# Performance work log

Hardware: AMD Instinct MI355X
Metric: run time of the kernel (lower is better)

The kernel has to match this reference:

```python
import jax, jax.numpy as jnp
import numpy as np
import math

B, H, N, D = 32, 8, 257, 64  # batch, heads, seq (256 patches + 1), head dim
DIM = H * D
PIX = 256  # 16*16 flattened mask pixels
EPS = 1e-5


def setup_inputs() -> dict:
    key = jax.random.key(0)
    k1, k2, k3 = jax.random.split(key, 3)
    x = jax.random.normal(k1, (B, N, DIM), dtype=jnp.float32)
    msk = jax.random.randint(k2, (B, 16, 16), 0, 128, dtype=jnp.int32)
    W_qkv = jax.random.normal(k3, (3 * DIM, DIM), dtype=jnp.float32) * (DIM ** -0.5)
    # past_kv initialized to identity per head (np.eye tiled in the torch forward)
    past_kv = jnp.broadcast_to(jnp.eye(D, dtype=jnp.float32), (B, H, D, D))
    gn_weight = jnp.ones((H,), dtype=jnp.float32)
    gn_bias = jnp.zeros((H,), dtype=jnp.float32)
    return {"x": x, "msk": msk, "W_qkv": W_qkv, "past_kv": past_kv,
            "gn_weight": gn_weight, "gn_bias": gn_bias}


def _build_mask(msk):
    # msk: [B,16,16] int; zeros replaced by pseudo-random ints in [1,128)
    noise = jax.random.randint(jax.random.key(42), msk.shape, 1, 128, dtype=jnp.int32)
    m = jnp.where(msk == 0, noise, msk).astype(jnp.float32)
    pix = m.reshape(B, PIX, 1)                       # [B,256,1]
    ip = pix @ jnp.swapaxes(pix, 1, 2)               # [B,256,256] outer product
    ip = ip / jnp.max(ip, axis=(1, 2), keepdims=True)
    dec0 = jnp.exp(-5.0 * jnp.linspace(0.0, 1.0, PIX))       # row [256]
    t = jnp.concatenate([jnp.broadcast_to(dec0[None, None, :], (B, 1, PIX)), ip], axis=1)  # [B,257,256]
    dec1 = jnp.exp(-5.0 * jnp.linspace(0.0, 1.0, N))         # col [257]
    t = jnp.concatenate([jnp.broadcast_to(dec1[None, :, None], (B, N, 1)), t], axis=2)     # [B,257,257]
    eye = jnp.eye(N, dtype=bool)
    t = jnp.where(eye, 1.0, t)   # fill_diagonal_(1)
    t = jnp.tril(t)
    return t[:, None, :, :]      # [B,1,N,N] broadcast over heads


def reference(x, msk, W_qkv, past_kv, gn_weight, gn_bias):
    scale = D ** -0.5  # decay_mask == chunk_decay == inner_decay == dim_heads**-0.5
    qkv = x @ W_qkv.T                                # [B,N,3*DIM]
    q, k, v = jnp.split(qkv, 3, axis=-1)
    def heads(t):
        return t.reshape(B, N, H, D).transpose(0, 2, 1, 3)  # b n (h d) -> b h n d
    q, k, v = heads(q), heads(k), heads(v)

    retention = jnp.einsum('bhnd,bhmd->bhnm', q, k) * scale
    weights_before = jax.nn.softmax(retention / math.sqrt(D), axis=-1)

    mask = _build_mask(msk)
    retention = retention * mask
    weights_after = jax.nn.softmax(retention / math.sqrt(D), axis=-1)

    inner_retention = jnp.einsum('bhnm,bhmd->bhnd', retention, v)
    cross_retention = jnp.einsum('bhnd,bhde->bhne', q, past_kv) * scale
    r = inner_retention + cross_retention            # [B,H,N,D]

    # GroupNorm(groups=H, channels=H): normalize each head over (N,D)
    mean = jnp.mean(r, axis=(2, 3), keepdims=True)
    var = jnp.mean((r - mean) ** 2, axis=(2, 3), keepdims=True)
    rn = (r - mean) / jnp.sqrt(var + EPS)
    rn = rn * gn_weight[None, :, None, None] + gn_bias[None, :, None, None]

    output = rn.transpose(0, 2, 1, 3).reshape(B, N, H * D)  # b h n d -> b n (h d)
    return (output, weights_before, weights_after)
```

## Files before the change

kernel.cpp:

```cpp
#include <hip/hip_runtime.h>
#include <stdint.h>

#define WB_OFF   4210688ull
#define WA_OFF   21119232ull

typedef short short8 __attribute__((ext_vector_type(8)));
typedef float floatx4 __attribute__((ext_vector_type(4)));
typedef __attribute__((address_space(1))) const unsigned int gu32;
typedef __attribute__((address_space(3))) unsigned int lu32;

#define RAW_BARRIER() do { \
  __builtin_amdgcn_sched_barrier(0); \
  asm volatile("s_waitcnt lgkmcnt(0)" ::: "memory"); \
  __builtin_amdgcn_s_barrier(); \
  __builtin_amdgcn_sched_barrier(0); \
} while(0)

__device__ __forceinline__ unsigned short f2bf(float f){
  union { float f; uint32_t u; } v; v.f = f;
  uint32_t u = v.u;
  uint32_t r = (u + 0x7FFFu + ((u >> 16) & 1u)) >> 16;
  return (unsigned short)r;
}

__device__ __forceinline__ void threefry(uint32_t k0, uint32_t k1, uint32_t c0, uint32_t c1,
                                         uint32_t& o0, uint32_t& o1){
  const uint32_t ks2 = k0 ^ k1 ^ 0x1BD11BDAu;
  uint32_t x0 = c0 + k0, x1 = c1 + k1;
#define TF_R4(a,b,c,d) \
  x0+=x1; x1=(x1<<(a))|(x1>>(32-(a))); x1^=x0; \
  x0+=x1; x1=(x1<<(b))|(x1>>(32-(b))); x1^=x0; \
  x0+=x1; x1=(x1<<(c))|(x1>>(32-(c))); x1^=x0; \
  x0+=x1; x1=(x1<<(d))|(x1>>(32-(d))); x1^=x0;
  TF_R4(13,15,26,6)  x0+=k1;  x1+=ks2+1u;
  TF_R4(17,29,16,24) x0+=ks2; x1+=k0+2u;
  TF_R4(13,15,26,6)  x0+=k0;  x1+=k1+3u;
  TF_R4(17,29,16,24) x0+=k1;  x1+=ks2+4u;
  TF_R4(13,15,26,6)  x0+=ks2; x1+=k0+5u;
#undef TF_R4
  o0 = x0; o1 = x1;
}

__global__ __launch_bounds__(256) void cvt_prep_kernel(const float* __restrict__ x,
                                                       const float* __restrict__ w,
                                                       unsigned short* __restrict__ xb,
                                                       unsigned short* __restrict__ wb,
                                                       const int* __restrict__ msk,
                                                       float* __restrict__ mnorm){
  __shared__ float sm[256];
  if (blockIdx.x < 4880){
    int i = blockIdx.x*256 + threadIdx.x;
    if (i < 1052672){
      float4 v = ((const float4*)x)[i];
      ushort4 o; o.x=f2bf(v.x); o.y=f2bf(v.y); o.z=f2bf(v.z); o.w=f2bf(v.w);
      ((ushort4*)xb)[i] = o;
    } else if (i < 1249280){
      int j = i - 1052672;
      float4 v = ((const float4*)w)[j];
      ushort4 o; o.x=f2bf(v.x); o.y=f2bf(v.y); o.z=f2bf(v.z); o.w=f2bf(v.w);
      ((ushort4*)wb)[j] = o;
    }
  } else {
    const int b = blockIdx.x - 4880, p = threadIdx.x;
    const int i = b*256 + p;
    uint32_t A0, A1, B0, B1;
    threefry(0u, 42u, 0u, 0u, A0, A1);
    threefry(0u, 42u, 0u, 1u, B0, B1);
    uint32_t h0, h1, l0, l1;
    threefry(A0, A1, 0u, (uint32_t)i, h0, h1);
    threefry(B0, B1, 0u, (uint32_t)i, l0, l1);
    uint32_t hb = h0 ^ h1, lb = l0 ^ l1;
    uint32_t off = ((hb % 127u) * 16u + (lb % 127u)) % 127u;
    int mv = msk[i];
    float m = (mv == 0) ? (float)(1u + off) : (float)mv;
    sm[p] = m; __syncthreads();
    for (int s = 128; s > 0; s >>= 1){
      if (p < s) sm[p] = fmaxf(sm[p], sm[p+s]);
      __syncthreads();
    }
    mnorm[i] = m / sm[0];
  }
}

__global__ __launch_bounds__(256) void qkv_gemm(const unsigned short* __restrict__ xb,
                                                const unsigned short* __restrict__ wb,
                                                unsigned short* __restrict__ qkv){
  __shared__ unsigned short sm2[128*64*2 + 128*8];
  unsigned short* al = sm2;
  unsigned short* bl = sm2 + 128*64;
  unsigned short* c_lds = sm2;
  const int bn = blockIdx.x, bm = blockIdx.y;
  const int tid = threadIdx.x;
  const int wave = tid >> 6, lane = tid & 63;
  const int l16 = lane & 15, lq = lane >> 4;
  const int wm = (wave & 1) * 64, wn = (wave >> 1) * 64;
  const int row0 = tid >> 3;
  const int ccg = ((tid & 7) ^ (row0 & 7)) * 8;
  const int sx = (l16 & 7);
  floatx4 acc[4][4] = {};
  for (int kk = 0; kk < 512; kk += 64){
    #pragma unroll
    for (int p = 0; p < 4; p++){
      int row = p*32 + row0;
      int gm = bm*128 + row; if (gm > 8223) gm = 8223;
      __builtin_amdgcn_global_load_lds((gu32*)&xb[(size_t)gm*512 + kk + ccg],
                                       (lu32*)&al[row*64 + (tid & 7)*8], 16, 0, 0);
      int gn = bn*128 + row;
      __builtin_amdgcn_global_load_lds((gu32*)&wb[(size_t)gn*512 + kk + ccg],
                                       (lu32*)&bl[row*64 + (tid & 7)*8], 16, 0, 0);
    }
    __syncthreads();
    #pragma unroll
    for (int ks = 0; ks < 2; ks++){
      short8 af[4], bf4[4];
      #pragma unroll
      for (int mi = 0; mi < 4; mi++){
        int ch = (ks*4 + lq) ^ sx;
        af[mi] = *(const short8*)&al[(wm + mi*16 + l16)*64 + ch*8];
      }
      #pragma unroll
      for (int ni = 0; ni < 4; ni++){
        int ch = (ks*4 + lq) ^ sx;
        bf4[ni] = *(const short8*)&bl[(wn + ni*16 + l16)*64 + ch*8];
      }
      #pragma unroll
      for (int mi = 0; mi < 4; mi++)
        #pragma unroll
        for (int ni = 0; ni < 4; ni++)
          acc[mi][ni] = __builtin_amdgcn_mfma_f32_16x16x32_bf16(af[mi], bf4[ni], acc[mi][ni], 0, 0, 0);
    }
    __syncthreads();
  }
  #pragma unroll
  for (int mi = 0; mi < 4; mi++)
    #pragma unroll
    for (int ni = 0; ni < 4; ni++)
      #pragma unroll
      for (int r = 0; r < 4; r++)
        c_lds[(wm + mi*16 + lq*4 + r)*136 + wn + ni*16 + l16] = f2bf(acc[mi][ni][r]);
  __syncthreads();
  for (int i = tid; i < 128*16; i += 256){
    int row = i >> 4, cc = (i & 15)*8;
    int gm = bm*128 + row;
    if (gm < 8224){
      ushort4 v0 = *(const ushort4*)&c_lds[row*136 + cc];
      ushort4 v1 = *(const ushort4*)&c_lds[row*136 + cc + 4];
      *(ushort4*)&qkv[(size_t)gm*1536 + bn*128 + cc] = v0;
      *(ushort4*)&qkv[(size_t)gm*1536 + bn*128 + cc + 4] = v1;
    }
  }
}

__global__ __launch_bounds__(256, 3) void retention_kernel(
    const unsigned short* __restrict__ qkv,
    const float* __restrict__ past_kv,
    const float* __restrict__ mnorm,
    float* __restrict__ out,
    float* __restrict__ partials){
  const int id = blockIdx.x;
  const int xcd = id & 7, slot = id >> 3;
  const int w_ = xcd*160 + slot;
  const int t  = w_ % 5;
  const int bh = w_ / 5;
  const int b = bh >> 3, h = bh & 7;
  const int tid = threadIdx.x;
  const int wave = tid >> 6, lane = tid & 63;
  const int l16 = lane & 15, lq = lane >> 4;
  const int rw = wave * 16;

  extern __shared__ unsigned char smem[];
  unsigned short* kl  = (unsigned short*)smem;
  unsigned short* vT  = (unsigned short*)smem;
  unsigned short* pkl = (unsigned short*)(smem + 39168);
  unsigned short* plw = (unsigned short*)(smem + 39168 + wave*1280);
  float* mn  = (float*)(smem + 48384);
  float* red = (float*)(smem + 49408);

  {
    uint32_t* z = (uint32_t*)(kl + 257*72);
    for (int i = tid; i < 540; i += 256) z[i] = 0;
  }
  ushort4 kreg[17];
  #pragma unroll
  for (int u = 0; u < 17; u++){
    int c = tid + u*256;
    if (c < 4112){
      int row = c >> 4, c4 = (c & 15) * 4;
      kreg[u] = *(const ushort4*)&qkv[(size_t)(b*257 + row)*1536 + 512 + h*64 + c4];
    }
  }
  float4 preg[4];
  #pragma unroll
  for (int u = 0; u < 4; u++){
    int c = tid + u*256;
    int d = c >> 4, e4 = (c & 15) * 4;
    preg[u] = *(const float4*)&past_kv[(size_t)bh*4096 + d*64 + e4];
  }
  float mnv = mnorm[b*256 + tid];
  int giA = t*64 + rw + l16; if (giA > 256) giA = 256;
  short8 aq[2];
  aq[0] = *(const short8*)&qkv[(size_t)(b*257 + giA)*1536 + h*64 + lq*8];
  aq[1] = *(const short8*)&qkv[(size_t)(b*257 + giA)*1536 + h*64 + 32 + lq*8];
  ushort4 vreg[17];
  #pragma unroll
  for (int u = 0; u < 17; u++){
    int c = tid + u*256;
    if (c < 4112){
      int row = c >> 4, c4 = (c & 15) * 4;
      vreg[u] = *(const ushort4*)&qkv[(size_t)(b*257 + row)*1536 + 1024 + h*64 + c4];
    }
  }
  #pragma unroll
  for (int u = 0; u < 17; u++){
    int c = tid + u*256;
    if (c < 4112){
      int row = c >> 4, c4 = (c & 15) * 4;
      *(ushort4*)&kl[row*72 + c4] = kreg[u];
    }
  }
  #pragma unroll
  for (int u = 0; u < 4; u++){
    int c = tid + u*256;
    int d = c >> 4, e4 = (c & 15) * 4;
    pkl[(e4+0)*72 + d] = f2bf(0.125f * preg[u].x);
    pkl[(e4+1)*72 + d] = f2bf(0.125f * preg[u].y);
    pkl[(e4+2)*72 + d] = f2bf(0.125f * preg[u].z);
    pkl[(e4+3)*72 + d] = f2bf(0.125f * preg[u].w);
  }
  mn[tid] = mnv;
  RAW_BARRIER();

  floatx4 acc2[4] = {};
  #pragma unroll
  for (int ks = 0; ks < 2; ks++)
    #pragma unroll
    for (int ni = 0; ni < 4; ni++){
      short8 bb = *(const short8*)&pkl[(ni*16 + l16)*72 + ks*32 + lq*8];
      acc2[ni] = __builtin_amdgcn_mfma_f32_16x16x32_bf16(aq[ks], bb, acc2[ni], 0, 0, 0);
    }

  floatx4 acc[17] = {};
  #pragma unroll
  for (int ks = 0; ks < 2; ks++)
    #pragma unroll
    for (int c = 0; c < 17; c++){
      short8 bb = *(const short8*)&kl[(c*16 + l16)*72 + ks*32 + lq*8];
      acc[c] = __builtin_amdgcn_mfma_f32_16x16x32_bf16(aq[ks], bb, acc[c], 0, 0, 0);
    }
  #pragma unroll
  for (int c = 0; c < 17; c++) acc[c] *= 0.125f;

  RAW_BARRIER();

  for (int i = tid; i < 64*19; i += 256){
    int row = i / 19, cc = (i % 19)*2 + 258;
    *(uint32_t*)&vT[row*296 + cc] = 0;
  }
  if (tid < 64) vT[tid*296 + 257] = 0;
  #pragma unroll
  for (int u = 0; u < 17; u++){
    int c = tid + u*256;
    if (c < 4112){
      int row = c >> 4, c4 = (c & 15) * 4;
      vT[(c4+0)*296 + row] = vreg[u].x;
      vT[(c4+1)*296 + row] = vreg[u].y;
      vT[(c4+2)*296 + row] = vreg[u].z;
      vT[(c4+3)*296 + row] = vreg[u].w;
    }
  }
  RAW_BARRIER();

  int gi[4]; bool rowok[4];
  #pragma unroll
  for (int r = 0; r < 4; r++){ gi[r] = t*64 + rw + lq*4 + r; rowok[r] = (gi[r] < 257); }

  float mx[4], sum_[4], inv_[4];

  #pragma unroll
  for (int r = 0; r < 4; r++) mx[r] = -3.0e38f;
  #pragma unroll
  for (int c = 0; c < 17; c++){
    bool jok = (c < 16) || (l16 == 0);
    if (jok){
      #pragma unroll
      for (int r = 0; r < 4; r++) mx[r] = fmaxf(mx[r], acc[c][r]);
    }
  }
  #pragma unroll
  for (int m = 1; m < 16; m <<= 1)
    #pragma unroll
    for (int r = 0; r < 4; r++) mx[r] = fmaxf(mx[r], __shfl_xor(mx[r], m, 64));
  #pragma unroll
  for (int r = 0; r < 4; r++) sum_[r] = 0.f;
  #pragma unroll
  for (int c = 0; c < 17; c++){
    bool jok = (c < 16) || (l16 == 0);
    if (jok){
      #pragma unroll
      for (int r = 0; r < 4; r++) sum_[r] += __expf((acc[c][r] - mx[r]) * 0.125f);
    }
  }
  #pragma unroll
  for (int m = 1; m < 16; m <<= 1)
    #pragma unroll
    for (int r = 0; r < 4; r++) sum_[r] += __shfl_xor(sum_[r], m, 64);
  #pragma unroll
  for (int r = 0; r < 4; r++) inv_[r] = 1.0f / sum_[r];

  {
    const size_t gbase = WB_OFF + (size_t)bh*66049;
    #pragma unroll
    for (int r = 0; r < 4; r++){
      size_t rb = gbase + (size_t)gi[r]*257;
      #pragma unroll
      for (int c = 0; c < 17; c++){
        int j = c*16 + l16;
        if (rowok[r] && j < 257){
          float v = __expf((acc[c][r] - mx[r]) * 0.125f) * inv_[r];
          __builtin_nontemporal_store(v, &out[rb + j]);
        }
      }
    }
  }

  #pragma unroll
  for (int c = 0; c < 17; c++){
    int j = c*16 + l16;
    #pragma unroll
    for (int r = 0; r < 4; r++){
      int ii = gi[r] > 256 ? 256 : gi[r];
      float mv;
      if (j > ii)       mv = 0.f;
      else if (j == ii) mv = 1.f;
      else if (j == 0)  mv = __expf(-5.f * (float)ii * (1.f/256.f));
      else              mv = mn[ii-1] * mn[j-1];
      acc[c][r] *= mv;
    }
  }

  #pragma unroll
  for (int r = 0; r < 4; r++) mx[r] = -3.0e38f;
  #pragma unroll
  for (int c = 0; c < 17; c++){
    bool jok = (c < 16) || (l16 == 0);
    if (jok){
      #pragma unroll
      for (int r = 0; r < 4; r++) mx[r] = fmaxf(mx[r], acc[c][r]);
    }
  }
  #pragma unroll
  for (int m = 1; m < 16; m <<= 1)
    #pragma unroll
    for (int r = 0; r < 4; r++) mx[r] = fmaxf(mx[r], __shfl_xor(mx[r], m, 64));
  #pragma unroll
  for (int r = 0; r < 4; r++) sum_[r] = 0.f;
  #pragma unroll
  for (int c = 0; c < 17; c++){
    bool jok = (c < 16) || (l16 == 0);
    if (jok){
      #pragma unroll
      for (int r = 0; r < 4; r++) sum_[r] += __expf((acc[c][r] - mx[r]) * 0.125f);
    }
  }
  #pragma unroll
  for (int m = 1; m < 16; m <<= 1)
    #pragma unroll
    for (int r = 0; r < 4; r++) sum_[r] += __shfl_xor(sum_[r], m, 64);
  #pragma unroll
  for (int r = 0; r < 4; r++) inv_[r] = 1.0f / sum_[r];

  {
    const size_t gbase = WA_OFF + (size_t)bh*66049;
    #pragma unroll
    for (int r = 0; r < 4; r++){
      size_t rb = gbase + (size_t)gi[r]*257;
      #pragma unroll
      for (int c = 0; c < 17; c++){
        int j = c*16 + l16;
        if (rowok[r] && j < 257){
          float v = __expf((acc[c][r] - mx[r]) * 0.125f) * inv_[r];
          __builtin_nontemporal_store(v, &out[rb + j]);
        }
      }
    }
  }

  const int nks = (t == 4) ? 9 : (2*t + 2);
  #pragma unroll
  for (int ks = 0; ks < 9; ks++){
    if (ks < nks){
      #pragma unroll
      for (int cc = 0; cc < 2; cc++){
        const int f = ks*2 + cc;
        #pragma unroll
        for (int r = 0; r < 4; r++){
          float val = (f < 17 && (f*16 + l16) < 257) ? acc[f][r] : 0.f;
          plw[(lq*4 + r)*40 + cc*16 + l16] = f2bf(val);
        }
      }
      short8 a = *(const short8*)&plw[l16*40 + lq*8];
      #pragma unroll
      for (int ni = 0; ni < 4; ni++){
        short8 bb = *(const short8*)&vT[(ni*16 + l16)*296 + ks*32 + lq*8];
        acc2[ni] = __builtin_amdgcn_mfma_f32_16x16x32_bf16(a, bb, acc2[ni], 0, 0, 0);
      }
    }
  }

  float ls = 0.f, lss = 0.f;
  #pragma unroll
  for (int ni = 0; ni < 4; ni++)
    #pragma unroll
    for (int r = 0; r < 4; r++)
      if (rowok[r]){
        float v = acc2[ni][r];
        ls += v; lss += v*v;
        out[(size_t)(b*257 + gi[r])*512 + h*64 + ni*16 + l16] = v;
      }
  #pragma unroll
  for (int m = 1; m < 64; m <<= 1){ ls += __shfl_xor(ls, m, 64); lss += __shfl_xor(lss, m, 64); }
  if (lane == 0){ red[wave*2] = ls; red[wave*2 + 1] = lss; }
  RAW_BARRIER();
  if (tid == 0){
    partials[((size_t)bh*5 + t)*2 + 0] = red[0] + red[2] + red[4] + red[6];
    partials[((size_t)bh*5 + t)*2 + 1] = red[1] + red[3] + red[5] + red[7];
  }
}

__global__ __launch_bounds__(256) void norm_kernel(const float* __restrict__ partials,
                                                   const float* __restrict__ gnw,
                                                   const float* __restrict__ gnb,
                                                   float* __restrict__ out){
  const int bh = blockIdx.x, b = bh >> 3, h = bh & 7;
  float s = 0.f, s2 = 0.f;
  #pragma unroll
  for (int tt = 0; tt < 5; tt++){
    s  += partials[(bh*5 + tt)*2 + 0];
    s2 += partials[(bh*5 + tt)*2 + 1];
  }
  const float cnt = 257.f * 64.f;
  float mean = s / cnt;
  float var  = s2 / cnt - mean * mean;
  float isd  = rsqrtf(var + 1e-5f);
  float wsc  = gnw[h] * isd;
  float bia  = gnb[h] - mean * wsc;
  for (int idx = threadIdx.x; idx < 257*16; idx += 256){
    int n = idx >> 4, e4 = (idx & 15) * 4;
    size_t off = (size_t)(b*257 + n)*512 + h*64 + e4;
    float4 v = *(float4*)&out[off];
    v.x = v.x * wsc + bia; v.y = v.y * wsc + bia;
    v.z = v.z * wsc + bia; v.w = v.w * wsc + bia;
    *(float4*)&out[off] = v;
  }
}

extern "C" void kernel_launch(void* const* d_in, const int* in_sizes, int n_in,
                              void* d_out, int out_size, void* d_ws, size_t ws_size,
                              hipStream_t stream){
  (void)in_sizes; (void)n_in; (void)out_size; (void)ws_size;
  const float* x   = (const float*)d_in[0];
  const int*   msk = (const int*)d_in[1];
  const float* w   = (const float*)d_in[2];
  const float* pkv = (const float*)d_in[3];
  const float* gnw = (const float*)d_in[4];
  const float* gnb = (const float*)d_in[5];
  float* out = (float*)d_out;

  unsigned short* qkv = (unsigned short*)d_ws;
  unsigned short* xb  = (unsigned short*)((char*)d_ws + 25264128);
  unsigned short* wb  = (unsigned short*)((char*)d_ws + 33685504);
  float* mnorm    = (float*)((char*)d_ws + 35258368);
  float* partials = (float*)((char*)d_ws + 35291136);

  hipLaunchKernelGGL(cvt_prep_kernel, dim3(4912), dim3(256), 0, stream,
                     x, w, xb, wb, msk, mnorm);
  hipLaunchKernelGGL(qkv_gemm, dim3(12, 65), dim3(256), 0, stream, xb, wb, qkv);
  hipLaunchKernelGGL(retention_kernel, dim3(1280), dim3(256), 49440, stream,
                     qkv, pkv, mnorm, out, partials);
  hipLaunchKernelGGL(norm_kernel, dim3(256), dim3(256), 0, stream, partials, gnw, gnb, out);
}
```

Baseline: 265.2 us.

## Stage K in two halves to shrink LDS and allow four blocks per CU

The retention kernel now loads K into LDS in two 128-row halves, with an extra barrier between the halves, instead of all 257 rows at once. The V-transpose stride also drops from 296 to 264, so the shared-memory footprint falls from 49440 to 39968 bytes. Launch bounds go from 3 to 4 blocks per CU to raise occupancy and hide latency. The trade-offs are an extra sync and LDS round, and a tighter register budget that may cause spills given the large kreg, vreg and acc register arrays.

```diff
diff --git a/kernel.cpp b/kernel.cpp
--- a/kernel.cpp
+++ b/kernel.cpp
@@ -151,7 +151,7 @@
   }
 }
 
-__global__ __launch_bounds__(256, 3) void retention_kernel(
+__global__ __launch_bounds__(256, 4) void retention_kernel(
     const unsigned short* __restrict__ qkv,
     const float* __restrict__ past_kv,
     const float* __restrict__ mnorm,
@@ -169,17 +169,13 @@
   const int rw = wave * 16;
 
   extern __shared__ unsigned char smem[];
-  unsigned short* kl  = (unsigned short*)smem;
+  unsigned short* klh = (unsigned short*)smem;
   unsigned short* vT  = (unsigned short*)smem;
-  unsigned short* pkl = (unsigned short*)(smem + 39168);
-  unsigned short* plw = (unsigned short*)(smem + 39168 + wave*1280);
-  float* mn  = (float*)(smem + 48384);
-  float* red = (float*)(smem + 49408);
-
-  {
-    uint32_t* z = (uint32_t*)(kl + 257*72);
-    for (int i = tid; i < 540; i += 256) z[i] = 0;
-  }
+  unsigned short* pkl = (unsigned short*)(smem + 20480);
+  unsigned short* plw = (unsigned short*)(smem + 33792 + wave*1280);
+  float* mn  = (float*)(smem + 38912);
+  float* red = (float*)(smem + 39936);
+
   ushort4 kreg[17];
   #pragma unroll
   for (int u = 0; u < 17; u++){
@@ -211,12 +207,10 @@
     }
   }
   #pragma unroll
-  for (int u = 0; u < 17; u++){
-    int c = tid + u*256;
-    if (c < 4112){
-      int row = c >> 4, c4 = (c & 15) * 4;
-      *(ushort4*)&kl[row*72 + c4] = kreg[u];
-    }
+  for (int u = 0; u < 8; u++){
+    int c = tid + u*256;
+    int row = c >> 4, c4 = (c & 15) * 4;
+    *(ushort4*)&klh[row*72 + c4] = kreg[u];
   }
   #pragma unroll
   for (int u = 0; u < 4; u++){
@@ -243,29 +237,49 @@
   #pragma unroll
   for (int ks = 0; ks < 2; ks++)
     #pragma unroll
-    for (int c = 0; c < 17; c++){
-      short8 bb = *(const short8*)&kl[(c*16 + l16)*72 + ks*32 + lq*8];
+    for (int c = 0; c < 8; c++){
+      short8 bb = *(const short8*)&klh[(c*16 + l16)*72 + ks*32 + lq*8];
       acc[c] = __builtin_amdgcn_mfma_f32_16x16x32_bf16(aq[ks], bb, acc[c], 0, 0, 0);
     }
-  #pragma unroll
-  for (int c = 0; c < 17; c++) acc[c] *= 0.125f;
-
-  RAW_BARRIER();
-
-  for (int i = tid; i < 64*19; i += 256){
-    int row = i / 19, cc = (i % 19)*2 + 258;
-    *(uint32_t*)&vT[row*296 + cc] = 0;
-  }
-  if (tid < 64) vT[tid*296 + 257] = 0;
-  #pragma unroll
-  for (int u = 0; u < 17; u++){
+  RAW_BARRIER();
+
+  #pragma unroll
+  for (int u = 8; u < 17; u++){
     int c = tid + u*256;
     if (c < 4112){
       int row = c >> 4, c4 = (c & 15) * 4;
-      vT[(c4+0)*296 + row] = vreg[u].x;
-      vT[(c4+1)*296 + row] = vreg[u].y;
-      vT[(c4+2)*296 + row] = vreg[u].z;
-      vT[(c4+3)*296 + row] = vreg[u].w;
+      *(ushort4*)&klh[(row-128)*72 + c4] = kreg[u];
+    }
+  }
+  RAW_BARRIER();
+
+  #pragma unroll
+  for (int ks = 0; ks < 2; ks++)
+    #pragma unroll
+    for (int c = 8; c < 17; c++){
+      const int rr = (c == 16) ? 128 : (c*16 - 128);
+      short8 bb = *(const short8*)&klh[(rr + ((c == 16) ? 0 : l16))*72 + ks*32 + lq*8];
+      acc[c] = __builtin_amdgcn_mfma_f32_16x16x32_bf16(aq[ks], bb, acc[c], 0, 0, 0);
+    }
+  #pragma unroll
+  for (int c = 0; c < 17; c++) acc[c] *= 0.125f;
+
+  RAW_BARRIER();
+
+  for (int i = tid; i < 448; i += 256){
+    int r = i / 7, cc = 257 + (i % 7);
+    vT[r*264 + cc] = 0;
+  }
+  if (tid < 16) ((uint32_t*)(smem + 33792))[tid] = 0;
+  #pragma unroll
+  for (int u = 0; u < 17; u++){
+    int c = tid + u*256;
+    if (c < 4112){
+      int row = c >> 4, c4 = (c & 15) * 4;
+      vT[(c4+0)*264 + row] = vreg[u].x;
+      vT[(c4+1)*264 + row] = vreg[u].y;
+      vT[(c4+2)*264 + row] = vreg[u].z;
+      vT[(c4+3)*264 + row] = vreg[u].w;
     }
   }
   RAW_BARRIER();
@@ -401,7 +415,7 @@
       short8 a = *(const short8*)&plw[l16*40 + lq*8];
       #pragma unroll
       for (int ni = 0; ni < 4; ni++){
-        short8 bb = *(const short8*)&vT[(ni*16 + l16)*296 + ks*32 + lq*8];
+        short8 bb = *(const short8*)&vT[(ni*16 + l16)*264 + ks*32 + lq*8];
         acc2[ni] = __builtin_amdgcn_mfma_f32_16x16x32_bf16(a, bb, acc2[ni], 0, 0, 0);
       }
     }
@@ -475,7 +489,7 @@
   hipLaunchKernelGGL(cvt_prep_kernel, dim3(4912), dim3(256), 0, stream,
                      x, w, xb, wb, msk, mnorm);
   hipLaunchKernelGGL(qkv_gemm, dim3(12, 65), dim3(256), 0, stream, xb, wb, qkv);
-  hipLaunchKernelGGL(retention_kernel, dim3(1280), dim3(256), 49440, stream,
+  hipLaunchKernelGGL(retention_kernel, dim3(1280), dim3(256), 39968, stream,
                      qkv, pkv, mnorm, out, partials);
   hipLaunchKernelGGL(norm_kernel, dim3(256), dim3(256), 0, stream, partials, gnw, gnb, out);
 }
```

Result: slower. 307.4 us (+15.9%).
